# Performance work log

Measured on AMD Instinct MI355X. Metric: run time of the kernel, lower is better.

Reference implementation:

```python
import jax, jax.numpy as jnp
import numpy as np

IN_FEATURES = 4096
LOCAL_FEATURES = 32
KERNEL_SIZE = 64
STRIDE = 1
PADDING = KERNEL_SIZE - 1
FOLD_NUM = (IN_FEATURES + PADDING - KERNEL_SIZE) // STRIDE + 1  # = 4096
BATCH = 256


def setup_inputs() -> dict:
    key = jax.random.key(0)
    k_x, k_w = jax.random.split(key, 2)
    x = jax.random.normal(k_x, (BATCH, IN_FEATURES), dtype=jnp.float32)
    # xavier_uniform over (kernel_size, local_features) fan dims
    limit = float(np.sqrt(6.0 / (KERNEL_SIZE + LOCAL_FEATURES)))
    weight = jax.random.uniform(
        k_w, (FOLD_NUM, KERNEL_SIZE, LOCAL_FEATURES),
        dtype=jnp.float32, minval=-limit, maxval=limit)
    bias = jnp.zeros((FOLD_NUM, LOCAL_FEATURES), dtype=jnp.float32)
    return {"x": x, "weight": weight, "bias": bias}


def reference(x, weight, bias):
    # pad right by kernel_size-1 with zeros (F.pad([0, padding]))
    xp = jnp.pad(x, ((0, 0), (0, PADDING)))
    # unfold: windows[b, f, k] = xp[b, f*stride + k]
    idx = jnp.arange(FOLD_NUM)[:, None] * STRIDE + jnp.arange(KERNEL_SIZE)[None, :]
    windows = xp[:, idx]  # [B, fold_num, kernel_size]
    # per-position matmul with unique weights + bias
    out = jnp.einsum('bfk,fkl->bfl', windows, weight) + bias  # [B, fold_num, local_features]
    return out
```

## Files before the change

kernel.cpp:

```cpp
#include <hip/hip_runtime.h>
#include <hip/hip_bf16.h>

#define IN_FEATURES   4096
#define LOCAL_FEATURES  32
#define KERNEL_SIZE     64
#define FOLD_NUM      4096
#define BATCH          256

#define XROW 4192
#define KPAD 96

using bf16 = __hip_bfloat16;
typedef __attribute__((ext_vector_type(8))) short bf16x8;
typedef __attribute__((ext_vector_type(4))) float f32x4;

static __device__ __forceinline__ short bfbits(float v) {
    __hip_bfloat16 h = __float2bfloat16(v);
    return *reinterpret_cast<short*>(&h);
}

__global__ void prep_kernel(const float* __restrict__ x, const float* __restrict__ w,
                            bf16* __restrict__ xb, bf16* __restrict__ wt) {
    __shared__ bf16 lds[2][32][KPAD];
    const int t = threadIdx.x;

    if (blockIdx.x >= 2048) {
        const int u   = (blockIdx.x - 2048) * 256 + t;
        const int row = u / 524;
        const int c8  = (u - row * 524) * 8;
        bf16x8 o;
        if (c8 < 4096) {
            const float4 a = *reinterpret_cast<const float4*>(x + (size_t)row * 4096 + c8);
            const float4 b = *reinterpret_cast<const float4*>(x + (size_t)row * 4096 + c8 + 4);
            o[0] = bfbits(a.x); o[1] = bfbits(a.y); o[2] = bfbits(a.z); o[3] = bfbits(a.w);
            o[4] = bfbits(b.x); o[5] = bfbits(b.y); o[6] = bfbits(b.z); o[7] = bfbits(b.w);
        } else {
            o = (bf16x8){0,0,0,0,0,0,0,0};
        }
        *reinterpret_cast<bf16x8*>(xb + (size_t)row * XROW + c8) = o;
        return;
    }

    const int f0 = blockIdx.x * 2;
    {
        uint4* z = reinterpret_cast<uint4*>(&lds[0][0][0]);
        const uint4 zz = {0, 0, 0, 0};
        z[t] = zz; z[t + 256] = zz; z[t + 512] = zz;
    }
    __syncthreads();
    {
        const int fp  = t >> 7;
        const int tt  = t & 127;
        const int shf = (f0 + fp) & 7;
        const float* src = w + (size_t)(f0 + fp) * 2048 + tt * 16;
        #pragma unroll
        for (int v = 0; v < 4; ++v) {
            const float4 val = *reinterpret_cast<const float4*>(src + v * 4);
            const int e  = tt * 16 + v * 4;
            const int k  = e >> 5;
            const int n0 = e & 31;
            lds[fp][n0 + 0][k + shf] = __float2bfloat16(val.x);
            lds[fp][n0 + 1][k + shf] = __float2bfloat16(val.y);
            lds[fp][n0 + 2][k + shf] = __float2bfloat16(val.z);
            lds[fp][n0 + 3][k + shf] = __float2bfloat16(val.w);
        }
    }
    __syncthreads();
    if (t < 192) {
        const int fp = t / 96;
        const int tt = t - fp * 96;
        const int n  = tt / 3;
        const int k0 = (tt - n * 3) * 32;
        const uint4* lp = reinterpret_cast<const uint4*>(&lds[fp][n][k0]);
        uint4* gp = reinterpret_cast<uint4*>(wt + ((size_t)(f0 + fp) * 32 + n) * KPAD + k0);
        gp[0] = lp[0]; gp[1] = lp[1]; gp[2] = lp[2]; gp[3] = lp[3];
    }
}

__global__ __launch_bounds__(256, 2)
void local_linear_main(const bf16* __restrict__ xb, const bf16* __restrict__ wt,
                       const float* __restrict__ bias, float* __restrict__ out)
{
    const int bid   = blockIdx.x;
    const int t     = threadIdx.x;
    const int lane  = t & 63;
    const int wid   = t >> 6;

    const int ftile = bid & 255;
    const int btile = bid >> 8;
    const int f0    = ftile * 16;
    const int fw    = f0 + wid * 4;
    const int base8 = fw & ~7;
    const int lrow  = lane & 15;
    const int kgrp  = lane >> 4;
    const int b0    = btile * 32;

    bf16x8 bfr[2][3];
    {
        const bf16* xbase = xb + base8 + kgrp * 8;
        #pragma unroll
        for (int bt = 0; bt < 2; ++bt)
            #pragma unroll
            for (int ks = 0; ks < 3; ++ks)
                bfr[bt][ks] = *reinterpret_cast<const bf16x8*>(
                    xbase + (size_t)(b0 + bt * 16 + lrow) * XROW + ks * 32);
    }

    f32x4 acc[4][2][2];
    #pragma unroll
    for (int i = 0; i < 4; ++i)
        #pragma unroll
        for (int mt = 0; mt < 2; ++mt)
            #pragma unroll
            for (int bt = 0; bt < 2; ++bt)
                acc[i][mt][bt] = (f32x4){0.f, 0.f, 0.f, 0.f};

    #pragma unroll
    for (int i = 0; i < 4; ++i) {
        const bf16* wbase = wt + (size_t)(fw + i) * (32 * KPAD) + kgrp * 8;
        bf16x8 afr[2][3];
        #pragma unroll
        for (int mt = 0; mt < 2; ++mt)
            #pragma unroll
            for (int ks = 0; ks < 3; ++ks)
                afr[mt][ks] = *reinterpret_cast<const bf16x8*>(
                    wbase + (mt * 16 + lrow) * KPAD + ks * 32);
        #pragma unroll
        for (int ks = 0; ks < 3; ++ks)
            #pragma unroll
            for (int mt = 0; mt < 2; ++mt)
                #pragma unroll
                for (int bt = 0; bt < 2; ++bt)
                    acc[i][mt][bt] = __builtin_amdgcn_mfma_f32_16x16x32_bf16(
                        afr[mt][ks], bfr[bt][ks], acc[i][mt][bt], 0, 0, 0);
    }

    #pragma unroll
    for (int i = 0; i < 4; ++i) {
        const int f = fw + i;
        #pragma unroll
        for (int mt = 0; mt < 2; ++mt) {
            const float4 bv = *reinterpret_cast<const float4*>(
                bias + f * 32 + mt * 16 + kgrp * 4);
            #pragma unroll
            for (int bt = 0; bt < 2; ++bt) {
                const size_t b = b0 + bt * 16 + lrow;
                float4 o;
                o.x = acc[i][mt][bt][0] + bv.x;
                o.y = acc[i][mt][bt][1] + bv.y;
                o.z = acc[i][mt][bt][2] + bv.z;
                o.w = acc[i][mt][bt][3] + bv.w;
                *reinterpret_cast<float4*>(
                    out + (b * FOLD_NUM + f) * 32 + mt * 16 + kgrp * 4) = o;
            }
        }
    }
}

#define LDA 80
#define LDB 80
__global__ __launch_bounds__(256, 2)
void local_linear_kernel(const float* __restrict__ x, const float* __restrict__ w,
                         const float* __restrict__ bias, float* __restrict__ out)
{
    __shared__ bf16 As[BATCH * LDA];
    __shared__ bf16 Bs[LOCAL_FEATURES * LDB];
    const int f = blockIdx.x, t = threadIdx.x, lane = t & 63, wid = t >> 6;
    {
        const int col = lane, gcol = f + col;
        const bool valid = (gcol < IN_FEATURES);
        const float* xp = x + gcol;
        #pragma unroll 8
        for (int i = 0; i < 64; ++i) {
            const int row = wid + i * 4;
            float v = valid ? xp[(size_t)row * IN_FEATURES] : 0.0f;
            As[row * LDA + col] = __float2bfloat16(v);
        }
    }
    {
        const float* wf = w + (size_t)f * (KERNEL_SIZE * LOCAL_FEATURES);
        #pragma unroll
        for (int v4 = 0; v4 < 2; ++v4) {
            const int e0 = (t + v4 * 256) * 4;
            const float4 val = *reinterpret_cast<const float4*>(wf + e0);
            const int k = e0 >> 5, n = e0 & 31;
            Bs[(n + 0) * LDB + k] = __float2bfloat16(val.x);
            Bs[(n + 1) * LDB + k] = __float2bfloat16(val.y);
            Bs[(n + 2) * LDB + k] = __float2bfloat16(val.z);
            Bs[(n + 3) * LDB + k] = __float2bfloat16(val.w);
        }
    }
    __syncthreads();
    f32x4 acc[4][2];
    #pragma unroll
    for (int mt = 0; mt < 4; ++mt)
        #pragma unroll
        for (int nt = 0; nt < 2; ++nt) acc[mt][nt] = (f32x4){0.f,0.f,0.f,0.f};
    const int lrow = lane & 15, kgrp = lane >> 4;
    #pragma unroll
    for (int ks = 0; ks < 2; ++ks) {
        const int kbase = ks * 32 + kgrp * 8;
        bf16x8 bfrag[2], afrag[4];
        #pragma unroll
        for (int nt = 0; nt < 2; ++nt)
            bfrag[nt] = *reinterpret_cast<const bf16x8*>(&Bs[(nt*16+lrow) * LDB + kbase]);
        #pragma unroll
        for (int mt = 0; mt < 4; ++mt)
            afrag[mt] = *reinterpret_cast<const bf16x8*>(&As[(wid*64+mt*16+lrow) * LDA + kbase]);
        #pragma unroll
        for (int mt = 0; mt < 4; ++mt)
            #pragma unroll
            for (int nt = 0; nt < 2; ++nt)
                acc[mt][nt] = __builtin_amdgcn_mfma_f32_16x16x32_bf16(
                    afrag[mt], bfrag[nt], acc[mt][nt], 0, 0, 0);
    }
    float bv[2];
    bv[0] = bias[f * 32 + lrow];
    bv[1] = bias[f * 32 + 16 + lrow];
    #pragma unroll
    for (int mt = 0; mt < 4; ++mt)
        #pragma unroll
        for (int nt = 0; nt < 2; ++nt) {
            const int n = nt * 16 + lrow;
            #pragma unroll
            for (int r = 0; r < 4; ++r) {
                const int b = wid * 64 + mt * 16 + kgrp * 4 + r;
                out[((size_t)b * FOLD_NUM + f) * 32 + n] = acc[mt][nt][r] + bv[nt];
            }
        }
}

extern "C" void kernel_launch(void* const* d_in, const int* in_sizes, int n_in,
                              void* d_out, int out_size, void* d_ws, size_t ws_size,
                              hipStream_t stream) {
    const float* x    = (const float*)d_in[0];
    const float* wgt  = (const float*)d_in[1];
    const float* bias = (const float*)d_in[2];
    float* out        = (float*)d_out;

    const size_t WS_X = (size_t)BATCH * XROW * sizeof(bf16);
    const size_t WS_W = (size_t)FOLD_NUM * 32 * KPAD * sizeof(bf16);

    if (ws_size >= WS_X + WS_W) {
        bf16* xb = (bf16*)d_ws;
        bf16* wt = (bf16*)((char*)d_ws + WS_X);
        prep_kernel<<<2048 + 524, 256, 0, stream>>>(x, wgt, xb, wt);
        local_linear_main<<<2048, 256, 0, stream>>>(xb, wt, bias, out);
    } else {
        local_linear_kernel<<<FOLD_NUM, 256, 0, stream>>>(x, wgt, bias, out);
    }
}
```

Measured before the change: 193.6 us.

## Stage output through LDS for coalesced nontemporal row stores and retile blocks

New measurement: 205.4 us. 1.06x slower.

```diff
diff --git a/kernel.cpp b/kernel.cpp
--- a/kernel.cpp
+++ b/kernel.cpp
@@ -9,6 +9,7 @@
 
 #define XROW 4192
 #define KPAD 96
+#define EROW 2052
 
 using bf16 = __hip_bfloat16;
 typedef __attribute__((ext_vector_type(8))) short bf16x8;
@@ -77,46 +78,43 @@
     }
 }
 
-__global__ __launch_bounds__(256, 2)
+__global__ __launch_bounds__(512, 3)
 void local_linear_main(const bf16* __restrict__ xb, const bf16* __restrict__ wt,
                        const float* __restrict__ bias, float* __restrict__ out)
 {
-    const int bid   = blockIdx.x;
-    const int t     = threadIdx.x;
-    const int lane  = t & 63;
-    const int wid   = t >> 6;
-
-    const int ftile = bid & 255;
-    const int btile = bid >> 8;
-    const int f0    = ftile * 16;
-    const int fw    = f0 + wid * 4;
-    const int base8 = fw & ~7;
-    const int lrow  = lane & 15;
-    const int kgrp  = lane >> 4;
-    const int b0    = btile * 32;
-
-    bf16x8 bfr[2][3];
-    {
-        const bf16* xbase = xb + base8 + kgrp * 8;
-        #pragma unroll
-        for (int bt = 0; bt < 2; ++bt)
-            #pragma unroll
-            for (int ks = 0; ks < 3; ++ks)
-                bfr[bt][ks] = *reinterpret_cast<const bf16x8*>(
-                    xbase + (size_t)(b0 + bt * 16 + lrow) * XROW + ks * 32);
-    }
-
-    f32x4 acc[4][2][2];
-    #pragma unroll
-    for (int i = 0; i < 4; ++i)
+    __shared__ float eld[4 * EROW];
+
+    const int bid  = blockIdx.x;
+    const int t    = threadIdx.x;
+    const int lane = t & 63;
+    const int wid  = t >> 6;
+
+    const int fg   = bid & 63;
+    const int bt   = bid >> 6;
+    const int f0   = fg * 64;
+    const int fw   = f0 + wid * 8;
+    const int lrow = lane & 15;
+    const int kgrp = lane >> 4;
+    const int b0   = bt * 16;
+    const int brow = b0 + lrow;
+
+    bf16x8 bfr[3];
+    {
+        const bf16* xbase = xb + (size_t)brow * XROW + fw + kgrp * 8;
+        #pragma unroll
+        for (int ks = 0; ks < 3; ++ks)
+            bfr[ks] = *reinterpret_cast<const bf16x8*>(xbase + ks * 32);
+    }
+
+    f32x4 acc[8][2];
+    #pragma unroll
+    for (int i = 0; i < 8; ++i)
         #pragma unroll
         for (int mt = 0; mt < 2; ++mt)
-            #pragma unroll
-            for (int bt = 0; bt < 2; ++bt)
-                acc[i][mt][bt] = (f32x4){0.f, 0.f, 0.f, 0.f};
-
-    #pragma unroll
-    for (int i = 0; i < 4; ++i) {
+            acc[i][mt] = (f32x4){0.f, 0.f, 0.f, 0.f};
+
+    #pragma unroll
+    for (int i = 0; i < 8; ++i) {
         const bf16* wbase = wt + (size_t)(fw + i) * (32 * KPAD) + kgrp * 8;
         bf16x8 afr[2][3];
         #pragma unroll
@@ -129,30 +127,42 @@
         for (int ks = 0; ks < 3; ++ks)
             #pragma unroll
             for (int mt = 0; mt < 2; ++mt)
-                #pragma unroll
-                for (int bt = 0; bt < 2; ++bt)
-                    acc[i][mt][bt] = __builtin_amdgcn_mfma_f32_16x16x32_bf16(
-                        afr[mt][ks], bfr[bt][ks], acc[i][mt][bt], 0, 0, 0);
-    }
-
-    #pragma unroll
-    for (int i = 0; i < 4; ++i) {
-        const int f = fw + i;
+                acc[i][mt] = __builtin_amdgcn_mfma_f32_16x16x32_bf16(
+                    afr[mt][ks], bfr[ks], acc[i][mt], 0, 0, 0);
+    }
+
+    #pragma unroll
+    for (int i = 0; i < 8; ++i)
         #pragma unroll
         for (int mt = 0; mt < 2; ++mt) {
             const float4 bv = *reinterpret_cast<const float4*>(
-                bias + f * 32 + mt * 16 + kgrp * 4);
-            #pragma unroll
-            for (int bt = 0; bt < 2; ++bt) {
-                const size_t b = b0 + bt * 16 + lrow;
-                float4 o;
-                o.x = acc[i][mt][bt][0] + bv.x;
-                o.y = acc[i][mt][bt][1] + bv.y;
-                o.z = acc[i][mt][bt][2] + bv.z;
-                o.w = acc[i][mt][bt][3] + bv.w;
-                *reinterpret_cast<float4*>(
-                    out + (b * FOLD_NUM + f) * 32 + mt * 16 + kgrp * 4) = o;
-            }
+                bias + (fw + i) * 32 + mt * 16 + kgrp * 4);
+            acc[i][mt][0] += bv.x; acc[i][mt][1] += bv.y;
+            acc[i][mt][2] += bv.z; acc[i][mt][3] += bv.w;
+        }
+
+    const size_t outcol0 = (size_t)f0 * 32;
+    #pragma unroll
+    for (int q = 0; q < 4; ++q) {
+        __syncthreads();
+        if ((lrow >> 2) == q) {
+            #pragma unroll
+            for (int i = 0; i < 8; ++i)
+                #pragma unroll
+                for (int mt = 0; mt < 2; ++mt)
+                    *reinterpret_cast<f32x4*>(
+                        &eld[(lrow & 3) * EROW + (wid * 8 + i) * 32 + mt * 16 + kgrp * 4])
+                        = acc[i][mt];
+        }
+        __syncthreads();
+        #pragma unroll
+        for (int j = 0; j < 4; ++j) {
+            const int Lf  = (j * 512 + t) * 4;
+            const int row = Lf >> 11;
+            const int col = Lf & 2047;
+            const f32x4 v = *reinterpret_cast<const f32x4*>(&eld[row * EROW + col]);
+            const size_t g = (size_t)(b0 + q * 4 + row) * (FOLD_NUM * 32) + outcol0 + col;
+            __builtin_nontemporal_store(v, reinterpret_cast<f32x4*>(out + g));
         }
     }
 }
@@ -245,7 +255,7 @@
         bf16* xb = (bf16*)d_ws;
         bf16* wt = (bf16*)((char*)d_ws + WS_X);
         prep_kernel<<<2048 + 524, 256, 0, stream>>>(x, wgt, xb, wt);
-        local_linear_main<<<2048, 256, 0, stream>>>(xb, wt, bias, out);
+        local_linear_main<<<1024, 512, 0, stream>>>(xb, wt, bias, out);
     } else {
         local_linear_kernel<<<FOLD_NUM, 256, 0, stream>>>(x, wgt, bias, out);
     }
```
